# Optimization experiments

Measured on AMD Instinct MI355X. Metric: run time of the kernel, lower is better.

Reference implementation:

```python
import jax, jax.numpy as jnp
import numpy as np
import math

L = 4      # layers / experts
AD = 512   # agent dim per layer
D = 512    # wsi_size / model dim
T = 64     # num_tokens
N = 4096   # WSI patches
NC = 2
PROJ = 256 # cosine gate projection dim
HID = 4 * D
CAP = math.ceil(T / L)  # top-1, capacity_factor=1.0
EPS = 1e-5
AUX_W = 0.01


def layer_norm(x, g, b):
    x32 = x.astype(jnp.float32)
    mu = x32.mean(-1, keepdims=True)
    var = x32.var(-1, keepdims=True)
    return ((x32 - mu) * jax.lax.rsqrt(var + EPS) * g + b).astype(x.dtype)


def mha(q_in, kv_in, w_qkv, b_qkv, w_out, b_out, n_heads):
    # torch nn.MultiheadAttention, unbatched (len, embed) inputs
    E = q_in.shape[-1]
    hd = E // n_heads
    wq, wk, wv = jnp.split(w_qkv, 3, axis=0)
    bq, bk, bv = jnp.split(b_qkv, 3)
    q = (q_in @ wq.T + bq).reshape(-1, n_heads, hd)
    k = (kv_in @ wk.T + bk).reshape(-1, n_heads, hd)
    v = (kv_in @ wv.T + bv).reshape(-1, n_heads, hd)
    scale = float(1.0 / np.sqrt(hd))
    attn = jax.nn.softmax(jnp.einsum('thd,shd->hts', q, k) * scale, axis=-1)
    out = jnp.einsum('hts,shd->thd', attn, v).reshape(-1, E)
    return out @ w_out.T + b_out


def moe_top1(x, proj_w, sim_mat, temp, w1, b1, w2, b2):
    # tutel cosine top-1 gate (fp32), capacity-limited batch-prioritized dispatch
    E = w1.shape[0]
    xf = x.astype(jnp.float32)
    p = xf @ proj_w                                             # [T, PROJ]
    p = p / (jnp.linalg.norm(p, axis=-1, keepdims=True) + 1e-8)
    s = sim_mat / (jnp.linalg.norm(sim_mat, axis=0, keepdims=True) + 1e-8)
    scale = jnp.exp(jnp.minimum(temp, jnp.log(jnp.float32(100.0))))
    logits = (p @ s) * scale                                    # [T, E]
    scores = jax.nn.softmax(logits, axis=-1)
    expert = jnp.argmax(logits, axis=-1)                        # [T]
    gate = jnp.take_along_axis(scores, expert[:, None], axis=1)[:, 0]
    # batch prioritized routing: higher-gate tokens claim capacity slots first
    order = jnp.argsort(-gate)
    oh = jax.nn.one_hot(expert[order], E, dtype=jnp.int32)
    pos_s = jnp.sum(jnp.cumsum(oh, axis=0) * oh, axis=1) - 1    # slot within expert
    inv = jnp.argsort(order)
    pos = pos_s[inv]
    keep = pos < CAP
    safe_pos = jnp.where(keep, pos, 0)
    # dispatch -> grouped expert FFN -> combine
    buf = jnp.zeros((E, CAP, x.shape[-1]), x.dtype)
    buf = buf.at[expert, safe_pos].add(jnp.where(keep[:, None], x, 0.0))
    h = jax.nn.gelu(jnp.einsum('ecd,edh->ech', buf, w1) + b1[:, None, :], approximate=False)
    y = jnp.einsum('ech,ehd->ecd', h, w2) + b2[:, None, :]
    out = y[expert, safe_pos] * (gate * keep)[:, None].astype(x.dtype)
    # load-balancing aux loss (top-1)
    me = scores.mean(0)
    ce = jax.nn.one_hot(expert, E, dtype=jnp.float32).mean(0)
    l_aux = jnp.sum(me * ce) * E
    return out, l_aux


def reference(share_feature, fet_tokens, ind_ln1_g, ind_ln1_b, ind_ln2_g, ind_ln2_b,
              ind_qkv_w, ind_qkv_b, ind_out_w, ind_out_b, ind_mlp_w, ind_mlp_b,
              gate_proj_w, gate_sim, gate_temp, exp_w1, exp_b1, exp_w2, exp_b2,
              gsa_ln1_g, gsa_ln1_b, gsa_qkv_w, gsa_qkv_b, gsa_out_w, gsa_out_b,
              gsa_ln2_g, gsa_ln2_b, gsa_fc_w, gsa_fc_b, gsa_proj_w, gsa_proj_b,
              butter_w, butter_b, cls_w, cls_b):
    cur = jnp.zeros((T, D), share_feature.dtype)
    feature1 = jnp.zeros((L, T, D), share_feature.dtype)
    aux = jnp.zeros((1,), jnp.float32)
    for i in range(L):  # small fixed per-layer loop (structurally distinct params)
        seg = share_feature[:, i * AD:(i + 1) * AD]
        sf = layer_norm(seg, ind_ln1_g[i], ind_ln1_b[i])
        tok = layer_norm(fet_tokens[i], ind_ln2_g[i], ind_ln2_b[i])
        attn_out = mha(tok, sf, ind_qkv_w[i], ind_qkv_b[i], ind_out_w[i], ind_out_b[i], AD)
        qf = attn_out @ ind_mlp_w[i].T + ind_mlp_b[i]   # [T, D]
        mo, la = moe_top1(qf, gate_proj_w, gate_sim, gate_temp, exp_w1, exp_b1, exp_w2, exp_b2)
        cur = cur + mo
        aux = aux + la * AUX_W
        feature1 = feature1.at[i].set(cur)
    cur = cur / L
    # GatedSFAttentionBlock (8 heads self-attn + QuickGELU MLP, pre-LN residual)
    x1 = layer_norm(cur, gsa_ln1_g, gsa_ln1_b)
    x = cur + mha(x1, x1, gsa_qkv_w, gsa_qkv_b, gsa_out_w, gsa_out_b, D // 64)
    x2 = layer_norm(x, gsa_ln2_g, gsa_ln2_b)
    h = x2 @ gsa_fc_w.T + gsa_fc_b
    h = h * jax.nn.sigmoid(1.702 * h)  # QuickGELU
    gated = x + (h @ gsa_proj_w.T + gsa_proj_b)
    # OutputBlock
    hb = (gated @ butter_w.T + butter_b).reshape(1, -1)  # [1, T*256]
    logits = hb @ cls_w.T + cls_b                        # [1, NC]
    Y_hat = jnp.argmax(logits, axis=1, keepdims=True)
    hazards = jax.nn.sigmoid(logits)
    feature2 = jnp.zeros((L, T, D), share_feature.dtype)
    feature2_pre = jnp.zeros((L, 1, NC), share_feature.dtype)
    return (logits, hazards, Y_hat, aux, feature1, feature2, feature2_pre)


def setup_inputs() -> dict:
    key = jax.random.key(0)
    ks = iter(jax.random.split(key, 40))
    def rn(shape, scale=0.02):
        return scale * jax.random.normal(next(ks), shape, dtype=jnp.float32)
    return dict(
        share_feature=jax.random.normal(next(ks), (N, L * AD), dtype=jnp.float32),
        fet_tokens=rn((L, T, AD), AD ** -0.5),
        ind_ln1_g=jnp.ones((L, AD)), ind_ln1_b=jnp.zeros((L, AD)),
        ind_ln2_g=jnp.ones((L, AD)), ind_ln2_b=jnp.zeros((L, AD)),
        ind_qkv_w=rn((L, 3 * AD, AD)), ind_qkv_b=jnp.zeros((L, 3 * AD)),
        ind_out_w=rn((L, AD, AD)), ind_out_b=jnp.zeros((L, AD)),
        ind_mlp_w=rn((L, D, AD)), ind_mlp_b=jnp.zeros((L, D)),
        gate_proj_w=rn((D, PROJ)), gate_sim=rn((PROJ, L)),
        gate_temp=jnp.asarray(np.log(10.0), jnp.float32),
        exp_w1=rn((L, D, HID)), exp_b1=jnp.zeros((L, HID)),
        exp_w2=rn((L, HID, D)), exp_b2=jnp.zeros((L, D)),
        gsa_ln1_g=jnp.ones((D,)), gsa_ln1_b=jnp.zeros((D,)),
        gsa_qkv_w=rn((3 * D, D)), gsa_qkv_b=jnp.zeros((3 * D,)),
        gsa_out_w=rn((D, D)), gsa_out_b=jnp.zeros((D,)),
        gsa_ln2_g=jnp.ones((D,)), gsa_ln2_b=jnp.zeros((D,)),
        gsa_fc_w=rn((4 * D, D)), gsa_fc_b=jnp.zeros((4 * D,)),
        gsa_proj_w=rn((D, 4 * D)), gsa_proj_b=jnp.zeros((D,)),
        butter_w=rn((256, D)), butter_b=jnp.zeros((256,)),
        cls_w=rn((NC, T * 256)), cls_b=jnp.zeros((NC,)),
    )
```

## Files before the change

### kernel.cpp

```cpp
#include <hip/hip_runtime.h>
#include <math.h>

#define LNUM 4
#define ADIM 512
#define TTOK 64
#define NSEQ 4096
#define HIDE 2048
#define CAPE 16
#define EPSV 1e-5f

typedef __bf16 bf16;
typedef bf16 bf16x8 __attribute__((ext_vector_type(8)));
typedef float f32x4 __attribute__((ext_vector_type(4)));

#define OFF_BUF   0
#define OFF_SSUM  (OFF_BUF  + 131072)
#define OFF_CNT   (OFF_SSUM + 16)
#define OFF_Q     (OFF_CNT  + 16)
#define OFF_AP    (OFF_Q    + 131072)
#define OFF_QF    (OFF_AP   + 131072)
#define OFF_P     (OFF_QF   + 131072)
#define OFF_QKV3  (OFF_P    + 65536)
#define OFF_XB    (OFF_QKV3 + 98304)
#define OFF_HROW  (OFF_XB   + 32768)
#define OFF_GTD   (OFF_HROW + 131072)
#define OFF_HB    (OFF_GTD  + 32768)
#define ZERO_N    (OFF_HB   + 16384)
#define OFF_KT    ZERO_N
#define OFF_VT    (OFF_KT   + LNUM*512*NSEQ)
#define OFF_KMAX  (OFF_VT   + LNUM*512*NSEQ)
#define OFF_KMIN  (OFF_KMAX + LNUM*512)
#define OFF_AO    (OFF_KMIN + LNUM*512)
#define OFF_GATE  (OFF_AO   + 131072)
#define OFF_EXP   (OFF_GATE + 256)
#define OFF_POS   (OFF_EXP  + 256)
#define OFF_KEEP  (OFF_POS  + 256)
#define OFF_HEXP  (OFF_KEEP + 256)
#define OFF_CUR   (OFF_HEXP + LNUM*4*CAPE*HIDE)
#define OFF_AO2   (OFF_CUR  + TTOK*512)
#define OFF_AH    (OFF_AO2  + TTOK*512)
#define OFF_AL    (OFF_AH + LNUM*NSEQ*256)
#define OFF_WH    (OFF_AL + LNUM*NSEQ*256)
#define OFF_WL    (OFF_WH + LNUM*1024*256)
#define OFF_YEXP  OFF_AH

#define O_F1   6
#define O_F2   (6 + LNUM*TTOK*512)
#define O_F2P  (O_F2 + LNUM*TTOK*512)

__device__ __forceinline__ float wave_sum(float v) {
#pragma unroll
  for (int o = 32; o > 0; o >>= 1) v += __shfl_down(v, o, 64);
  return v;
}
__device__ __forceinline__ float wave_sum_all(float v) {
#pragma unroll
  for (int o = 32; o > 0; o >>= 1) v += __shfl_xor(v, o, 64);
  return v;
}
__device__ __forceinline__ float block_sum256(float v) {
  __shared__ float r[4];
  v = wave_sum(v);
  int wid = threadIdx.x >> 6, lane = threadIdx.x & 63;
  if (lane == 0) r[wid] = v;
  __syncthreads();
  float s = r[0] + r[1] + r[2] + r[3];
  __syncthreads();
  return s;
}

__global__ void k_zero(float* __restrict__ p, int n) {
  int i = blockIdx.x * 256 + threadIdx.x;
  if (i < n) p[i] = 0.f;
}

__global__ __launch_bounds__(64) void k_cvt_a(const float* __restrict__ SF,
      const float* __restrict__ G, const float* __restrict__ Bta,
      bf16* __restrict__ AH, bf16* __restrict__ AL) {
  int row = blockIdx.x;
  int l = row >> 12, m = row & 4095;
  int lane = threadIdx.x;
  const float* src = SF + (size_t)m * (LNUM * ADIM) + l * ADIM;
  float4 a = *(const float4*)(src + lane * 8);
  float4 b = *(const float4*)(src + lane * 8 + 4);
  float sum = (a.x + a.y) + (a.z + a.w) + (b.x + b.y) + (b.z + b.w);
  float sq = a.x*a.x + a.y*a.y + a.z*a.z + a.w*a.w + b.x*b.x + b.y*b.y + b.z*b.z + b.w*b.w;
  sum = wave_sum_all(sum); sq = wave_sum_all(sq);
  float mu = sum * (1.f / 512.f);
  float rs = rsqrtf(sq * (1.f / 512.f) - mu * mu + EPSV);
  float4 g0 = *(const float4*)(G + l * 512 + lane * 8);
  float4 g1 = *(const float4*)(G + l * 512 + lane * 8 + 4);
  float4 c0 = *(const float4*)(Bta + l * 512 + lane * 8);
  float4 c1 = *(const float4*)(Bta + l * 512 + lane * 8 + 4);
  float x[8];
  x[0] = (a.x - mu) * rs * g0.x + c0.x;  x[1] = (a.y - mu) * rs * g0.y + c0.y;
  x[2] = (a.z - mu) * rs * g0.z + c0.z;  x[3] = (a.w - mu) * rs * g0.w + c0.w;
  x[4] = (b.x - mu) * rs * g1.x + c1.x;  x[5] = (b.y - mu) * rs * g1.y + c1.y;
  x[6] = (b.z - mu) * rs * g1.z + c1.z;  x[7] = (b.w - mu) * rs * g1.w + c1.w;
  bf16x8 vh, vl;
#pragma unroll
  for (int j = 0; j < 8; j++) {
    bf16 h = (bf16)x[j];
    vh[j] = h;
    vl[j] = (bf16)(x[j] - (float)h);
  }
  *(bf16x8*)(AH + (size_t)row * 512 + lane * 8) = vh;
  *(bf16x8*)(AL + (size_t)row * 512 + lane * 8) = vl;
}

__global__ __launch_bounds__(64) void k_cvt_w(const float* __restrict__ Wqkv,
      bf16* __restrict__ WH, bf16* __restrict__ WL) {
  int row = blockIdx.x;
  int l = row >> 10, r = row & 1023;
  int lane = threadIdx.x;
  const float* src = Wqkv + (size_t)l * 1536 * 512 + (size_t)(512 + r) * 512 + lane * 8;
  float4 a = *(const float4*)(src);
  float4 b = *(const float4*)(src + 4);
  float x[8] = {a.x, a.y, a.z, a.w, b.x, b.y, b.z, b.w};
  bf16x8 vh, vl;
#pragma unroll
  for (int j = 0; j < 8; j++) {
    bf16 h = (bf16)x[j];
    vh[j] = h;
    vl[j] = (bf16)(x[j] - (float)h);
  }
  *(bf16x8*)(WH + (size_t)row * 512 + lane * 8) = vh;
  *(bf16x8*)(WL + (size_t)row * 512 + lane * 8) = vl;
}

__global__ __launch_bounds__(256) void k_mfma_kv(
      const bf16* __restrict__ AH, const bf16* __restrict__ AL,
      const bf16* __restrict__ WH, const bf16* __restrict__ WL,
      const float* __restrict__ Bqkv,
      float* __restrict__ KT, float* __restrict__ VT) {
  __shared__ bf16 sAh[128*32], sAl[128*32], sWh[128*32], sWl[128*32];
  int l = blockIdx.z;
  int n0 = blockIdx.x * 128, m0 = blockIdx.y * 128;
  int tid = threadIdx.x;
  int lane = tid & 63;
  int w = tid >> 6;
  int wm = w >> 1, wn = w & 1;
  const bf16* gAh = AH + ((size_t)l * 4096 + m0) * 512;
  const bf16* gAl = AL + ((size_t)l * 4096 + m0) * 512;
  const bf16* gWh = WH + ((size_t)l * 1024 + n0) * 512;
  const bf16* gWl = WL + ((size_t)l * 1024 + n0) * 512;
  int ch0 = tid * 2, ch1 = tid * 2 + 1;
  int r0 = ch0 >> 2, q0 = (ch0 & 3) * 8;
  int r1 = ch1 >> 2, q1 = (ch1 & 3) * 8;
  int fr = lane & 15, fq = (lane >> 4) * 8;
  f32x4 acc[4][4] = {};
  for (int k0 = 0; k0 < 512; k0 += 32) {
    *(bf16x8*)&sAh[r0*32 + q0] = *(const bf16x8*)&gAh[(size_t)r0*512 + k0 + q0];
    *(bf16x8*)&sAh[r1*32 + q1] = *(const bf16x8*)&gAh[(size_t)r1*512 + k0 + q1];
    *(bf16x8*)&sAl[r0*32 + q0] = *(const bf16x8*)&gAl[(size_t)r0*512 + k0 + q0];
    *(bf16x8*)&sAl[r1*32 + q1] = *(const bf16x8*)&gAl[(size_t)r1*512 + k0 + q1];
    *(bf16x8*)&sWh[r0*32 + q0] = *(const bf16x8*)&gWh[(size_t)r0*512 + k0 + q0];
    *(bf16x8*)&sWh[r1*32 + q1] = *(const bf16x8*)&gWh[(size_t)r1*512 + k0 + q1];
    *(bf16x8*)&sWl[r0*32 + q0] = *(const bf16x8*)&gWl[(size_t)r0*512 + k0 + q0];
    *(bf16x8*)&sWl[r1*32 + q1] = *(const bf16x8*)&gWl[(size_t)r1*512 + k0 + q1];
    __syncthreads();
    bf16x8 ah[4], al[4], bh[4], bl[4];
#pragma unroll
    for (int i = 0; i < 4; i++) {
      ah[i] = *(const bf16x8*)&sAh[(wm*64 + i*16 + fr)*32 + fq];
      al[i] = *(const bf16x8*)&sAl[(wm*64 + i*16 + fr)*32 + fq];
      bh[i] = *(const bf16x8*)&sWh[(wn*64 + i*16 + fr)*32 + fq];
      bl[i] = *(const bf16x8*)&sWl[(wn*64 + i*16 + fr)*32 + fq];
    }
#pragma unroll
    for (int i = 0; i < 4; i++)
#pragma unroll
      for (int j = 0; j < 4; j++) {
        acc[i][j] = __builtin_amdgcn_mfma_f32_16x16x32_bf16(ah[i], bh[j], acc[i][j], 0, 0, 0);
        acc[i][j] = __builtin_amdgcn_mfma_f32_16x16x32_bf16(ah[i], bl[j], acc[i][j], 0, 0, 0);
        acc[i][j] = __builtin_amdgcn_mfma_f32_16x16x32_bf16(al[i], bh[j], acc[i][j], 0, 0, 0);
      }
    __syncthreads();
  }
#pragma unroll
  for (int j = 0; j < 4; j++) {
    int n = n0 + wn*64 + j*16 + fr;
    float bias = Bqkv[l * 1536 + 512 + n];
    float* base = (n < 512) ? (KT + ((size_t)(l*512 + n)) * 4096)
                            : (VT + ((size_t)(l*512 + n - 512)) * 4096);
#pragma unroll
    for (int i = 0; i < 4; i++) {
      int mb = m0 + wm*64 + i*16 + (lane >> 4) * 4;
      float4 o = make_float4(acc[i][j][0] + bias, acc[i][j][1] + bias,
                             acc[i][j][2] + bias, acc[i][j][3] + bias);
      *(float4*)(base + mb) = o;
    }
  }
}

__global__ __launch_bounds__(256) void k_minmax(const float* __restrict__ KT,
                                                float* __restrict__ kmax, float* __restrict__ kmin) {
  int row = blockIdx.x;
  const float4* k = (const float4*)(KT + (size_t)row * 4096);
  float mx = -3.4e38f, mn = 3.4e38f;
  for (int i = threadIdx.x; i < 1024; i += 256) {
    float4 v = k[i];
    mx = fmaxf(mx, fmaxf(fmaxf(v.x, v.y), fmaxf(v.z, v.w)));
    mn = fminf(mn, fminf(fminf(v.x, v.y), fminf(v.z, v.w)));
  }
#pragma unroll
  for (int o = 32; o > 0; o >>= 1) {
    mx = fmaxf(mx, __shfl_down(mx, o, 64));
    mn = fminf(mn, __shfl_down(mn, o, 64));
  }
  __shared__ float rmx[4], rmn[4];
  int wid = threadIdx.x >> 6, lane = threadIdx.x & 63;
  if (lane == 0) { rmx[wid] = mx; rmn[wid] = mn; }
  __syncthreads();
  if (threadIdx.x == 0) {
    kmax[row] = fmaxf(fmaxf(rmx[0], rmx[1]), fmaxf(rmx[2], rmx[3]));
    kmin[row] = fminf(fminf(rmn[0], rmn[1]), fminf(rmn[2], rmn[3]));
  }
}

__global__ __launch_bounds__(64) void k_ln(const float* __restrict__ IN,
      const float* __restrict__ G, const float* __restrict__ B,
      float* __restrict__ OUT, int gstride) {
  int t = blockIdx.x, l = blockIdx.y;
  int row = l * 64 + t;
  int lane = threadIdx.x;
  const float* x = IN + (size_t)row * 512 + lane * 8;
  float4 a = ((const float4*)x)[0], b = ((const float4*)x)[1];
  float sum = (a.x + a.y) + (a.z + a.w) + (b.x + b.y) + (b.z + b.w);
  float sq = a.x*a.x + a.y*a.y + a.z*a.z + a.w*a.w + b.x*b.x + b.y*b.y + b.z*b.z + b.w*b.w;
  sum = wave_sum_all(sum); sq = wave_sum_all(sq);
  float mu = sum * (1.f / 512.f);
  float rs = rsqrtf(sq * (1.f / 512.f) - mu * mu + EPSV);
  const float* gp = G + l * gstride + lane * 8;
  const float* bp = B + l * gstride + lane * 8;
  float4 g0 = ((const float4*)gp)[0], g1 = ((const float4*)gp)[1];
  float4 c0 = ((const float4*)bp)[0], c1 = ((const float4*)bp)[1];
  float4 o0, o1;
  o0.x = (a.x - mu) * rs * g0.x + c0.x;  o0.y = (a.y - mu) * rs * g0.y + c0.y;
  o0.z = (a.z - mu) * rs * g0.z + c0.z;  o0.w = (a.w - mu) * rs * g0.w + c0.w;
  o1.x = (b.x - mu) * rs * g1.x + c1.x;  o1.y = (b.y - mu) * rs * g1.y + c1.y;
  o1.z = (b.z - mu) * rs * g1.z + c1.z;  o1.w = (b.w - mu) * rs * g1.w + c1.w;
  float* op = OUT + (size_t)row * 512 + lane * 8;
  ((float4*)op)[0] = o0; ((float4*)op)[1] = o1;
}

__global__ __launch_bounds__(256) void k_gemm64(
      const float* __restrict__ IN, const float* __restrict__ W,
      const float* __restrict__ BIAS, const float* __restrict__ RES,
      float* __restrict__ OUT, int K, int N, long wl, int bl) {
  int l = blockIdx.z;
  int n0 = blockIdx.x * 64;
  int kc0 = blockIdx.y * 128;
  const float* INl = IN + (size_t)l * 64 * K;
  const float* Wl  = W + (size_t)l * wl;
  float* OUTl = OUT + (size_t)l * 64 * N;
  __shared__ float sA[64][68], sB[64][68];
  int tid = threadIdx.x;
  int tx = tid & 15, ty = tid >> 4;
  float acc[4][4];
  if (blockIdx.y == 0) {
#pragma unroll
    for (int j = 0; j < 4; j++) {
      float bv = BIAS ? BIAS[bl * l + n0 + tx*4 + j] : 0.f;
#pragma unroll
      for (int i = 0; i < 4; i++)
        acc[i][j] = bv + (RES ? RES[((size_t)l*64 + ty*4 + i) * N + n0 + tx*4 + j] : 0.f);
    }
  } else {
#pragma unroll
    for (int i = 0; i < 4; i++)
#pragma unroll
      for (int j = 0; j < 4; j++) acc[i][j] = 0.f;
  }
  for (int kc = kc0; kc < kc0 + 128; kc += 64) {
    for (int i = tid; i < 1024; i += 256) {
      int r = i >> 4;
      int kq = i & 15;
      float4 av = *(const float4*)(INl + (size_t)r * K + kc + kq*4);
      sA[kq*4+0][r] = av.x; sA[kq*4+1][r] = av.y; sA[kq*4+2][r] = av.z; sA[kq*4+3][r] = av.w;
      float4 bv = *(const float4*)(Wl + (size_t)(n0 + r) * K + kc + kq*4);
      sB[kq*4+0][r] = bv.x; sB[kq*4+1][r] = bv.y; sB[kq*4+2][r] = bv.z; sB[kq*4+3][r] = bv.w;
    }
    __syncthreads();
#pragma unroll 8
    for (int kk = 0; kk < 64; kk++) {
      float4 a4 = *(const float4*)&sA[kk][ty*4];
      float4 b4 = *(const float4*)&sB[kk][tx*4];
      float a[4] = {a4.x,a4.y,a4.z,a4.w}, b[4] = {b4.x,b4.y,b4.z,b4.w};
#pragma unroll
      for (int i = 0; i < 4; i++)
#pragma unroll
        for (int j = 0; j < 4; j++) acc[i][j] = fmaf(a[i], b[j], acc[i][j]);
    }
    __syncthreads();
  }
#pragma unroll
  for (int i = 0; i < 4; i++)
#pragma unroll
    for (int j = 0; j < 4; j++)
      atomicAdd(&OUTl[(size_t)(ty*4+i) * N + n0 + tx*4 + j], acc[i][j]);
}

__global__ __launch_bounds__(256) void k_gemm64t(
      const float* __restrict__ IN, const float* __restrict__ W,
      float* __restrict__ OUT, int K, int N) {
  int l = blockIdx.z;
  int n0 = blockIdx.x * 64;
  int kc0 = blockIdx.y * 128;
  const float* INl = IN + (size_t)l * 64 * K;
  float* OUTl = OUT + (size_t)l * 64 * N;
  __shared__ float sA[64][68], sB[64][68];
  int tid = threadIdx.x;
  int tx = tid & 15, ty = tid >> 4;
  float acc[4][4] = {};
  for (int kc = kc0; kc < kc0 + 128; kc += 64) {
    for (int i = tid; i < 1024; i += 256) {
      int r = i >> 4;
      int kq = i & 15;
      float4 av = *(const float4*)(INl + (size_t)r * K + kc + kq*4);
      sA[kq*4+0][r] = av.x; sA[kq*4+1][r] = av.y; sA[kq*4+2][r] = av.z; sA[kq*4+3][r] = av.w;
      float4 bv = *(const float4*)(W + (size_t)(kc + r) * N + n0 + kq*4);
      *(float4*)&sB[r][kq*4] = bv;
    }
    __syncthreads();
#pragma unroll 8
    for (int kk = 0; kk < 64; kk++) {
      float4 a4 = *(const float4*)&sA[kk][ty*4];
      float4 b4 = *(const float4*)&sB[kk][tx*4];
      float a[4] = {a4.x,a4.y,a4.z,a4.w}, b[4] = {b4.x,b4.y,b4.z,b4.w};
#pragma unroll
      for (int i = 0; i < 4; i++)
#pragma unroll
        for (int j = 0; j < 4; j++) acc[i][j] = fmaf(a[i], b[j], acc[i][j]);
    }
    __syncthreads();
  }
#pragma unroll
  for (int i = 0; i < 4; i++)
#pragma unroll
    for (int j = 0; j < 4; j++)
      atomicAdd(&OUTl[(size_t)(ty*4+i) * N + n0 + tx*4 + j], acc[i][j]);
}

__global__ __launch_bounds__(256) void k_attn(const float* __restrict__ KT, const float* __restrict__ VT,
      const float* __restrict__ Q, const float* __restrict__ kmax, const float* __restrict__ kmin,
      float* __restrict__ AO) {
  int h = blockIdx.x, l = blockIdx.y;
  int tid = threadIdx.x;
  int w = tid >> 6, t = tid & 63;
  __shared__ float pden[4][64], pnum[4][64];
  const float* kp = KT + ((size_t)(l * 512 + h)) * 4096 + w * 1024;
  const float* vp = VT + ((size_t)(l * 512 + h)) * 4096 + w * 1024;
  float q = Q[((size_t)l * TTOK + t) * 512 + h];
  float km = kmax[l * 512 + h], kn = kmin[l * 512 + h];
  float m = (q >= 0.f) ? q * km : q * kn;
  float d0 = 0.f, d1 = 0.f, n0 = 0.f, n1 = 0.f;
  for (int s = 0; s < 1024; s += 8) {
    float4 ka = *(const float4*)(kp + s), kb = *(const float4*)(kp + s + 4);
    float4 va = *(const float4*)(vp + s), vb = *(const float4*)(vp + s + 4);
    float e;
    e = __expf(fmaf(q, ka.x, -m)); d0 += e; n0 = fmaf(e, va.x, n0);
    e = __expf(fmaf(q, ka.y, -m)); d1 += e; n1 = fmaf(e, va.y, n1);
    e = __expf(fmaf(q, ka.z, -m)); d0 += e; n0 = fmaf(e, va.z, n0);
    e = __expf(fmaf(q, ka.w, -m)); d1 += e; n1 = fmaf(e, va.w, n1);
    e = __expf(fmaf(q, kb.x, -m)); d0 += e; n0 = fmaf(e, vb.x, n0);
    e = __expf(fmaf(q, kb.y, -m)); d1 += e; n1 = fmaf(e, vb.y, n1);
    e = __expf(fmaf(q, kb.z, -m)); d0 += e; n0 = fmaf(e, vb.z, n0);
    e = __expf(fmaf(q, kb.w, -m)); d1 += e; n1 = fmaf(e, vb.w, n1);
  }
  pden[w][t] = d0 + d1; pnum[w][t] = n0 + n1;
  __syncthreads();
  if (w == 0) {
    float d = pden[0][t] + pden[1][t] + pden[2][t] + pden[3][t];
    float n = pnum[0][t] + pnum[1][t] + pnum[2][t] + pnum[3][t];
    AO[((size_t)l * TTOK + t) * 512 + h] = n / d;
  }
}

__global__ __launch_bounds__(64) void k_gate2(const float* __restrict__ P,
      const float* __restrict__ SIM, const float* __restrict__ TEMP,
      float* __restrict__ gate, int* __restrict__ expert,
      float* __restrict__ ssum, int* __restrict__ cnt) {
  int t = blockIdx.x, l = blockIdx.y;
  int lane = threadIdx.x;
  float4 p4 = *(const float4*)(P + ((size_t)(l * 64 + t)) * 256 + lane * 4);
  float ss = p4.x*p4.x + p4.y*p4.y + p4.z*p4.z + p4.w*p4.w;
  ss = wave_sum_all(ss);
  float invp = 1.f / (sqrtf(ss) + 1e-8f);
  float le[4] = {}, ne[4] = {};
#pragma unroll
  for (int j = 0; j < 4; j++) {
    float pv = (j == 0) ? p4.x : (j == 1) ? p4.y : (j == 2) ? p4.z : p4.w;
    float4 s4 = *(const float4*)(SIM + (size_t)(lane * 4 + j) * 4);
    le[0] = fmaf(pv, s4.x, le[0]); le[1] = fmaf(pv, s4.y, le[1]);
    le[2] = fmaf(pv, s4.z, le[2]); le[3] = fmaf(pv, s4.w, le[3]);
    ne[0] = fmaf(s4.x, s4.x, ne[0]); ne[1] = fmaf(s4.y, s4.y, ne[1]);
    ne[2] = fmaf(s4.z, s4.z, ne[2]); ne[3] = fmaf(s4.w, s4.w, ne[3]);
  }
#pragma unroll
  for (int e = 0; e < 4; e++) { le[e] = wave_sum_all(le[e]); ne[e] = wave_sum_all(ne[e]); }
  if (lane == 0) {
    float scale = __expf(fminf(TEMP[0], 4.6051701859880914f));
    float lg[4];
#pragma unroll
    for (int e = 0; e < 4; e++) lg[e] = le[e] * invp / (sqrtf(ne[e]) + 1e-8f) * scale;
    int best = 0; float bv = lg[0];
    if (lg[1] > bv) { best = 1; bv = lg[1]; }
    if (lg[2] > bv) { best = 2; bv = lg[2]; }
    if (lg[3] > bv) { best = 3; bv = lg[3]; }
    float mx = fmaxf(fmaxf(lg[0], lg[1]), fmaxf(lg[2], lg[3]));
    float e0 = __expf(lg[0]-mx), e1 = __expf(lg[1]-mx), e2 = __expf(lg[2]-mx), e3 = __expf(lg[3]-mx);
    float inv = 1.f / (e0 + e1 + e2 + e3);
    float s0 = e0*inv, s1 = e1*inv, s2 = e2*inv, s3 = e3*inv;
    float sb = (best == 0) ? s0 : (best == 1) ? s1 : (best == 2) ? s2 : s3;
    gate[l * TTOK + t] = sb;
    expert[l * TTOK + t] = best;
    atomicAdd(&ssum[l*4+0], s0); atomicAdd(&ssum[l*4+1], s1);
    atomicAdd(&ssum[l*4+2], s2); atomicAdd(&ssum[l*4+3], s3);
    atomicAdd(&cnt[l*4+best], 1);
  }
}

__global__ __launch_bounds__(64) void k_route(const float* __restrict__ gate, const int* __restrict__ expert,
                                              int* __restrict__ pos, int* __restrict__ keep) {
  int l = blockIdx.x;
  int t = threadIdx.x;
  __shared__ float g[64];
  __shared__ int e[64];
  g[t] = gate[l * TTOK + t]; e[t] = expert[l * TTOK + t];
  __syncthreads();
  float gt = g[t]; int et = e[t];
  int p = 0;
  for (int u = 0; u < 64; u++)
    if (e[u] == et && (g[u] > gt || (g[u] == gt && u < t))) p++;
  pos[l * TTOK + t] = p;
  keep[l * TTOK + t] = (p < CAPE) ? 1 : 0;
}

__global__ __launch_bounds__(128) void k_scatter(const float* __restrict__ QF, const int* __restrict__ expert,
      const int* __restrict__ pos, const int* __restrict__ keep, float* __restrict__ buf) {
  int t = blockIdx.x, l = blockIdx.y;
  int idx = l * TTOK + t;
  if (!keep[idx]) return;
  int e = expert[idx], p = pos[idx];
  const float4* src = (const float4*)(QF + ((size_t)l * TTOK + t) * 512);
  float4* dst = (float4*)(buf + (((size_t)(l * 4 + e)) * CAPE + p) * 512);
  dst[threadIdx.x] = src[threadIdx.x];
}

__global__ __launch_bounds__(256) void k_moe_h(const float* __restrict__ buf, const float* __restrict__ W1,
      const float* __restrict__ B1, float* __restrict__ H) {
  int le = blockIdx.y;
  int e = le & 3;
  int col = blockIdx.x * 256 + threadIdx.x;
  const float* act = buf + (size_t)le * 16 * 512;
  const float* wp = W1 + (size_t)e * 512 * HIDE + col;
  float acc[16];
#pragma unroll
  for (int c = 0; c < 16; c++) acc[c] = 0.f;
  for (int k0 = 0; k0 < 512; k0 += 4) {
    float4 a[16];
#pragma unroll
    for (int c = 0; c < 16; c++) a[c] = *(const float4*)(act + c * 512 + k0);
#pragma unroll
    for (int j = 0; j < 4; j++) {
      float wv = wp[(size_t)(k0 + j) * HIDE];
#pragma unroll
      for (int c = 0; c < 16; c++) acc[c] = fmaf(((const float*)&a[c])[j], wv, acc[c]);
    }
  }
  float bias = B1[e * HIDE + col];
  float* outp = H + (size_t)le * 16 * HIDE + col;
#pragma unroll
  for (int c = 0; c < 16; c++) {
    float v = acc[c] + bias;
    outp[(size_t)c * HIDE] = 0.5f * v * (1.f + erff(v * 0.70710678118654752f));
  }
}

__global__ __launch_bounds__(256) void k_moe_y(const float* __restrict__ H, const float* __restrict__ W2,
      const float* __restrict__ B2, float* __restrict__ Y) {
  int le = blockIdx.y;
  int e = le & 3;
  int cl = threadIdx.x & 63, kq = threadIdx.x >> 6;
  int col = blockIdx.x * 64 + cl;
  const float* act = H + (size_t)le * 16 * HIDE + kq * 512;
  const float* wp = W2 + (size_t)e * HIDE * 512 + (size_t)(kq * 512) * 512 + col;
  float acc[16];
#pragma unroll
  for (int c = 0; c < 16; c++) acc[c] = 0.f;
  for (int k0 = 0; k0 < 512; k0 += 4) {
    float4 a[16];
#pragma unroll
    for (int c = 0; c < 16; c++) a[c] = *(const float4*)(act + c * HIDE + k0);
#pragma unroll
    for (int j = 0; j < 4; j++) {
      float wv = wp[(size_t)(k0 + j) * 512];
#pragma unroll
      for (int c = 0; c < 16; c++) acc[c] = fmaf(((const float*)&a[c])[j], wv, acc[c]);
    }
  }
  __shared__ float sacc[4][16][64];
#pragma unroll
  for (int c = 0; c < 16; c++) sacc[kq][c][cl] = acc[c];
  __syncthreads();
  if (kq == 0) {
    float bias = B2[e * 512 + col];
#pragma unroll
    for (int c = 0; c < 16; c++) {
      float tot = sacc[0][c][cl] + sacc[1][c][cl] + sacc[2][c][cl] + sacc[3][c][cl] + bias;
      Y[(size_t)le * 16 * 512 + (size_t)c * 512 + col] = tot;
    }
  }
}

__global__ __launch_bounds__(512) void k_combine(const float* __restrict__ Y, const int* __restrict__ expert,
      const int* __restrict__ pos, const int* __restrict__ keep, const float* __restrict__ gate,
      float* __restrict__ f1, float* __restrict__ f2, float* __restrict__ cur) {
  int t = blockIdx.x;
  int d = threadIdx.x;
  float acc = 0.f;
#pragma unroll
  for (int l = 0; l < LNUM; l++) {
    int idx = l * TTOK + t;
    float v = 0.f;
    if (keep[idx]) {
      int e = expert[idx], p = pos[idx];
      v = Y[(((size_t)(l * 4 + e)) * CAPE + p) * 512 + d] * gate[idx];
    }
    acc += v;
    f1[((size_t)l * TTOK + t) * 512 + d] = acc;
    f2[((size_t)l * TTOK + t) * 512 + d] = 0.f;
  }
  cur[(size_t)t * 512 + d] = acc * 0.25f;
}

__global__ __launch_bounds__(256) void k_gsa_attn(const float* __restrict__ QKV3, float* __restrict__ AO2) {
  int h = blockIdx.x;
  __shared__ float qh[64][65], kh[64][65], vh[64][65];
  __shared__ float ps[4][64];
  for (int i = threadIdx.x; i < 4096; i += 256) {
    int t = i >> 6, d = i & 63;
    qh[t][d] = QKV3[(size_t)t * 1536 + h * 64 + d];
    kh[t][d] = QKV3[(size_t)t * 1536 + 512 + h * 64 + d];
    vh[t][d] = QKV3[(size_t)t * 1536 + 1024 + h * 64 + d];
  }
  __syncthreads();
  int w = threadIdx.x >> 6, lane = threadIdx.x & 63;
  for (int tt = 0; tt < 16; tt++) {
    int t = w * 16 + tt;
    float acc = 0.f;
#pragma unroll 8
    for (int d = 0; d < 64; d++) acc = fmaf(qh[t][d], kh[lane][d], acc);
    acc *= 0.125f;
    float m = acc;
#pragma unroll
    for (int o = 32; o > 0; o >>= 1) m = fmaxf(m, __shfl_xor(m, o, 64));
    float e = __expf(acc - m);
    float den = e;
#pragma unroll
    for (int o = 32; o > 0; o >>= 1) den += __shfl_xor(den, o, 64);
    ps[w][lane] = e / den;
    __syncthreads();
    float o2 = 0.f;
#pragma unroll 8
    for (int s = 0; s < 64; s++) o2 = fmaf(ps[w][s], vh[s][lane], o2);
    AO2[(size_t)t * 512 + h * 64 + lane] = o2;
    __syncthreads();
  }
}

__global__ __launch_bounds__(256) void k_swish(float* __restrict__ H) {
  int i = blockIdx.x * 256 + threadIdx.x;
  float x = H[i];
  H[i] = x / (1.f + __expf(-1.702f * x));
}

__global__ __launch_bounds__(256) void k_final(const float* __restrict__ HB,
      const float* __restrict__ CW, const float* __restrict__ CB,
      const float* __restrict__ ssum, const int* __restrict__ cnt,
      float* __restrict__ out) {
  int tid = threadIdx.x;
  float p0 = 0.f, p1 = 0.f;
  for (int i = tid; i < 16384; i += 256) {
    float h = HB[i];
    p0 = fmaf(h, CW[i], p0);
    p1 = fmaf(h, CW[16384 + i], p1);
  }
  p0 = block_sum256(p0);
  p1 = block_sum256(p1);
  if (tid == 0) {
    float l0 = p0 + CB[0], l1 = p1 + CB[1];
    out[0] = l0; out[1] = l1;
    out[2] = 1.f / (1.f + __expf(-l0));
    out[3] = 1.f / (1.f + __expf(-l1));
    out[4] = (l1 > l0) ? 1.f : 0.f;
    float aux = 0.f;
    for (int i = 0; i < 16; i++) aux += (ssum[i] * (1.f / 64.f)) * ((float)cnt[i] * (1.f / 64.f));
    out[5] = aux * 4.f * 0.01f;
  }
  if (tid < 8) out[O_F2P + tid] = 0.f;
}

extern "C" void kernel_launch(void* const* d_in, const int* in_sizes, int n_in,
                              void* d_out, int out_size, void* d_ws, size_t ws_size,
                              hipStream_t stream) {
  const float* SF    = (const float*)d_in[0];
  const float* TOK   = (const float*)d_in[1];
  const float* LN1G  = (const float*)d_in[2];
  const float* LN1B  = (const float*)d_in[3];
  const float* LN2G  = (const float*)d_in[4];
  const float* LN2B  = (const float*)d_in[5];
  const float* QKVW  = (const float*)d_in[6];
  const float* QKVB  = (const float*)d_in[7];
  const float* OUTW  = (const float*)d_in[8];
  const float* OUTB  = (const float*)d_in[9];
  const float* MLPW  = (const float*)d_in[10];
  const float* MLPB  = (const float*)d_in[11];
  const float* GPW   = (const float*)d_in[12];
  const float* GSIM  = (const float*)d_in[13];
  const float* GTMP  = (const float*)d_in[14];
  const float* EW1   = (const float*)d_in[15];
  const float* EB1   = (const float*)d_in[16];
  const float* EW2   = (const float*)d_in[17];
  const float* EB2   = (const float*)d_in[18];
  const float* GL1G  = (const float*)d_in[19];
  const float* GL1B  = (const float*)d_in[20];
  const float* GQKVW = (const float*)d_in[21];
  const float* GQKVB = (const float*)d_in[22];
  const float* GOUTW = (const float*)d_in[23];
  const float* GOUTB = (const float*)d_in[24];
  const float* GL2G  = (const float*)d_in[25];
  const float* GL2B  = (const float*)d_in[26];
  const float* GFCW  = (const float*)d_in[27];
  const float* GFCB  = (const float*)d_in[28];
  const float* GPJW  = (const float*)d_in[29];
  const float* GPJB  = (const float*)d_in[30];
  const float* BTW   = (const float*)d_in[31];
  const float* BTB   = (const float*)d_in[32];
  const float* CLW   = (const float*)d_in[33];
  const float* CLB   = (const float*)d_in[34];

  float* ws  = (float*)d_ws;
  float* out = (float*)d_out;

  float* BUF  = ws + OFF_BUF;
  float* SSUM = ws + OFF_SSUM;
  int*   CNT  = (int*)(ws + OFF_CNT);
  float* Q    = ws + OFF_Q;
  float* AP   = ws + OFF_AP;
  float* QF   = ws + OFF_QF;
  float* P    = ws + OFF_P;
  float* QKV3 = ws + OFF_QKV3;
  float* XB   = ws + OFF_XB;
  float* HROW = ws + OFF_HROW;
  float* GTD  = ws + OFF_GTD;
  float* HBB  = ws + OFF_HB;
  float* KT   = ws + OFF_KT;
  float* VT   = ws + OFF_VT;
  float* KMAX = ws + OFF_KMAX;
  float* KMIN = ws + OFF_KMIN;
  float* AOSH = ws + OFF_AO;
  float* GATE = ws + OFF_GATE;
  int*   EXPI = (int*)(ws + OFF_EXP);
  int*   POSI = (int*)(ws + OFF_POS);
  int*   KEEPI= (int*)(ws + OFF_KEEP);
  float* HEXP = ws + OFF_HEXP;
  float* CUR  = ws + OFF_CUR;
  float* AO2  = ws + OFF_AO2;
  bf16*  AH   = (bf16*)(ws + OFF_AH);
  bf16*  AL   = (bf16*)(ws + OFF_AL);
  bf16*  WH   = (bf16*)(ws + OFF_WH);
  bf16*  WL   = (bf16*)(ws + OFF_WL);
  float* YEXP = ws + OFF_YEXP;

  k_zero<<<(ZERO_N + 255) / 256, 256, 0, stream>>>(ws, ZERO_N);
  k_cvt_a<<<LNUM * NSEQ, 64, 0, stream>>>(SF, LN1G, LN1B, AH, AL);
  k_cvt_w<<<LNUM * 1024, 64, 0, stream>>>(QKVW, WH, WL);
  k_mfma_kv<<<dim3(8, 32, LNUM), 256, 0, stream>>>(AH, AL, WH, WL, QKVB, KT, VT);
  k_minmax<<<LNUM * 512, 256, 0, stream>>>(KT, KMAX, KMIN);
  k_ln<<<dim3(TTOK, LNUM), 64, 0, stream>>>(TOK, LN2G, LN2B, AOSH, 512);
  k_gemm64<<<dim3(8, 4, LNUM), 256, 0, stream>>>(AOSH, QKVW, QKVB, nullptr, Q, 512, 512, 1536L*512, 1536);
  k_attn<<<dim3(512, LNUM), 256, 0, stream>>>(KT, VT, Q, KMAX, KMIN, AOSH);
  k_gemm64<<<dim3(8, 4, LNUM), 256, 0, stream>>>(AOSH, OUTW, OUTB, nullptr, AP, 512, 512, 512L*512, 512);
  k_gemm64<<<dim3(8, 4, LNUM), 256, 0, stream>>>(AP, MLPW, MLPB, nullptr, QF, 512, 512, 512L*512, 512);
  k_gemm64t<<<dim3(4, 4, LNUM), 256, 0, stream>>>(QF, GPW, P, 512, 256);
  k_gate2<<<dim3(TTOK, LNUM), 64, 0, stream>>>(P, GSIM, GTMP, GATE, EXPI, SSUM, CNT);
  k_route<<<LNUM, 64, 0, stream>>>(GATE, EXPI, POSI, KEEPI);
  k_scatter<<<dim3(TTOK, LNUM), 128, 0, stream>>>(QF, EXPI, POSI, KEEPI, BUF);
  k_moe_h<<<dim3(8, 16), 256, 0, stream>>>(BUF, EW1, EB1, HEXP);
  k_moe_y<<<dim3(8, 16), 256, 0, stream>>>(HEXP, EW2, EB2, YEXP);
  k_combine<<<TTOK, 512, 0, stream>>>(YEXP, EXPI, POSI, KEEPI, GATE, out + O_F1, out + O_F2, CUR);
  k_ln<<<dim3(TTOK, 1), 64, 0, stream>>>(CUR, GL1G, GL1B, AOSH, 0);
  k_gemm64<<<dim3(24, 4, 1), 256, 0, stream>>>(AOSH, GQKVW, GQKVB, nullptr, QKV3, 512, 1536, 0, 0);
  k_gsa_attn<<<8, 256, 0, stream>>>(QKV3, AO2);
  k_gemm64<<<dim3(8, 4, 1), 256, 0, stream>>>(AO2, GOUTW, GOUTB, CUR, XB, 512, 512, 0, 0);
  k_ln<<<dim3(TTOK, 1), 64, 0, stream>>>(XB, GL2G, GL2B, AOSH, 0);
  k_gemm64<<<dim3(32, 4, 1), 256, 0, stream>>>(AOSH, GFCW, GFCB, nullptr, HROW, 512, 2048, 0, 0);
  k_swish<<<(TTOK * HIDE) / 256, 256, 0, stream>>>(HROW);
  k_gemm64<<<dim3(8, 16, 1), 256, 0, stream>>>(HROW, GPJW, GPJB, XB, GTD, 2048, 512, 0, 0);
  k_gemm64<<<dim3(4, 4, 1), 256, 0, stream>>>(GTD, BTW, BTB, nullptr, HBB, 512, 256, 0, 0);
  k_final<<<1, 256, 0, stream>>>(HBB, CLW, CLB, SSUM, CNT, out);
}
```

Baseline: 818.3 us.

## Fuse min/max into attention, merge MoE gating kernels, fuse swish into GEMM

Computes K min/max inside the attention kernel, which now keeps K/V in registers and loops over tokens with exp2, so the separate min/max pass and its extra read of K are gone. Merges the gate, route and scatter kernels into one per-layer block. Fuses swish into a non-split GEMM epilogue, removing the separate swish kernel. Also swaps the MFMA grid axes to change block scheduling order. Fewer launches and less memory traffic, at the cost of less parallelism in the fused gate kernel and the unsplit FC GEMM.

```diff
diff --git a/kernel.cpp b/kernel.cpp
--- a/kernel.cpp
+++ b/kernel.cpp
@@ -8,6 +8,7 @@
 #define HIDE 2048
 #define CAPE 16
 #define EPSV 1e-5f
+#define LOG2E 1.44269504088896340736f
 
 typedef __bf16 bf16;
 typedef bf16 bf16x8 __attribute__((ext_vector_type(8)));
@@ -28,9 +29,7 @@
 #define ZERO_N    (OFF_HB   + 16384)
 #define OFF_KT    ZERO_N
 #define OFF_VT    (OFF_KT   + LNUM*512*NSEQ)
-#define OFF_KMAX  (OFF_VT   + LNUM*512*NSEQ)
-#define OFF_KMIN  (OFF_KMAX + LNUM*512)
-#define OFF_AO    (OFF_KMIN + LNUM*512)
+#define OFF_AO    (OFF_VT   + LNUM*512*NSEQ)
 #define OFF_GATE  (OFF_AO   + 131072)
 #define OFF_EXP   (OFF_GATE + 256)
 #define OFF_POS   (OFF_EXP  + 256)
@@ -135,7 +134,7 @@
       float* __restrict__ KT, float* __restrict__ VT) {
   __shared__ bf16 sAh[128*32], sAl[128*32], sWh[128*32], sWl[128*32];
   int l = blockIdx.z;
-  int n0 = blockIdx.x * 128, m0 = blockIdx.y * 128;
+  int m0 = blockIdx.x * 128, n0 = blockIdx.y * 128;
   int tid = threadIdx.x;
   int lane = tid & 63;
   int w = tid >> 6;
@@ -190,31 +189,6 @@
                              acc[i][j][2] + bias, acc[i][j][3] + bias);
       *(float4*)(base + mb) = o;
     }
-  }
-}
-
-__global__ __launch_bounds__(256) void k_minmax(const float* __restrict__ KT,
-                                                float* __restrict__ kmax, float* __restrict__ kmin) {
-  int row = blockIdx.x;
-  const float4* k = (const float4*)(KT + (size_t)row * 4096);
-  float mx = -3.4e38f, mn = 3.4e38f;
-  for (int i = threadIdx.x; i < 1024; i += 256) {
-    float4 v = k[i];
-    mx = fmaxf(mx, fmaxf(fmaxf(v.x, v.y), fmaxf(v.z, v.w)));
-    mn = fminf(mn, fminf(fminf(v.x, v.y), fminf(v.z, v.w)));
-  }
-#pragma unroll
-  for (int o = 32; o > 0; o >>= 1) {
-    mx = fmaxf(mx, __shfl_down(mx, o, 64));
-    mn = fminf(mn, __shfl_down(mn, o, 64));
-  }
-  __shared__ float rmx[4], rmn[4];
-  int wid = threadIdx.x >> 6, lane = threadIdx.x & 63;
-  if (lane == 0) { rmx[wid] = mx; rmn[wid] = mn; }
-  __syncthreads();
-  if (threadIdx.x == 0) {
-    kmax[row] = fmaxf(fmaxf(rmx[0], rmx[1]), fmaxf(rmx[2], rmx[3]));
-    kmin[row] = fminf(fminf(rmn[0], rmn[1]), fminf(rmn[2], rmn[3]));
   }
 }
 
@@ -247,10 +221,12 @@
 __global__ __launch_bounds__(256) void k_gemm64(
       const float* __restrict__ IN, const float* __restrict__ W,
       const float* __restrict__ BIAS, const float* __restrict__ RES,
-      float* __restrict__ OUT, int K, int N, long wl, int bl) {
+      float* __restrict__ OUT, int K, int N, long wl, int bl, int act) {
   int l = blockIdx.z;
   int n0 = blockIdx.x * 64;
-  int kc0 = blockIdx.y * 128;
+  bool split = (gridDim.y > 1);
+  int kcBeg = blockIdx.y * 128;
+  int kcEnd = split ? kcBeg + 128 : K;
   const float* INl = IN + (size_t)l * 64 * K;
   const float* Wl  = W + (size_t)l * wl;
   float* OUTl = OUT + (size_t)l * 64 * N;
@@ -272,7 +248,7 @@
 #pragma unroll
       for (int j = 0; j < 4; j++) acc[i][j] = 0.f;
   }
-  for (int kc = kc0; kc < kc0 + 128; kc += 64) {
+  for (int kc = kcBeg; kc < kcEnd; kc += 64) {
     for (int i = tid; i < 1024; i += 256) {
       int r = i >> 4;
       int kq = i & 15;
@@ -294,11 +270,22 @@
     }
     __syncthreads();
   }
-#pragma unroll
-  for (int i = 0; i < 4; i++)
-#pragma unroll
-    for (int j = 0; j < 4; j++)
-      atomicAdd(&OUTl[(size_t)(ty*4+i) * N + n0 + tx*4 + j], acc[i][j]);
+  if (split) {
+#pragma unroll
+    for (int i = 0; i < 4; i++)
+#pragma unroll
+      for (int j = 0; j < 4; j++)
+        atomicAdd(&OUTl[(size_t)(ty*4+i) * N + n0 + tx*4 + j], acc[i][j]);
+  } else {
+#pragma unroll
+    for (int i = 0; i < 4; i++)
+#pragma unroll
+      for (int j = 0; j < 4; j++) {
+        float o = acc[i][j];
+        if (act == 1) o = o / (1.f + __expf(-1.702f * o));
+        OUTl[(size_t)(ty*4+i) * N + n0 + tx*4 + j] = o;
+      }
+  }
 }
 
 __global__ __launch_bounds__(256) void k_gemm64t(
@@ -343,63 +330,102 @@
 }
 
 __global__ __launch_bounds__(256) void k_attn(const float* __restrict__ KT, const float* __restrict__ VT,
-      const float* __restrict__ Q, const float* __restrict__ kmax, const float* __restrict__ kmin,
-      float* __restrict__ AO) {
+      const float* __restrict__ Q, float* __restrict__ AO) {
   int h = blockIdx.x, l = blockIdx.y;
   int tid = threadIdx.x;
-  int w = tid >> 6, t = tid & 63;
-  __shared__ float pden[4][64], pnum[4][64];
-  const float* kp = KT + ((size_t)(l * 512 + h)) * 4096 + w * 1024;
-  const float* vp = VT + ((size_t)(l * 512 + h)) * 4096 + w * 1024;
-  float q = Q[((size_t)l * TTOK + t) * 512 + h];
-  float km = kmax[l * 512 + h], kn = kmin[l * 512 + h];
-  float m = (q >= 0.f) ? q * km : q * kn;
-  float d0 = 0.f, d1 = 0.f, n0 = 0.f, n1 = 0.f;
-  for (int s = 0; s < 1024; s += 8) {
-    float4 ka = *(const float4*)(kp + s), kb = *(const float4*)(kp + s + 4);
-    float4 va = *(const float4*)(vp + s), vb = *(const float4*)(vp + s + 4);
-    float e;
-    e = __expf(fmaf(q, ka.x, -m)); d0 += e; n0 = fmaf(e, va.x, n0);
-    e = __expf(fmaf(q, ka.y, -m)); d1 += e; n1 = fmaf(e, va.y, n1);
-    e = __expf(fmaf(q, ka.z, -m)); d0 += e; n0 = fmaf(e, va.z, n0);
-    e = __expf(fmaf(q, ka.w, -m)); d1 += e; n1 = fmaf(e, va.w, n1);
-    e = __expf(fmaf(q, kb.x, -m)); d0 += e; n0 = fmaf(e, vb.x, n0);
-    e = __expf(fmaf(q, kb.y, -m)); d1 += e; n1 = fmaf(e, vb.y, n1);
-    e = __expf(fmaf(q, kb.z, -m)); d0 += e; n0 = fmaf(e, vb.z, n0);
-    e = __expf(fmaf(q, kb.w, -m)); d1 += e; n1 = fmaf(e, vb.w, n1);
-  }
-  pden[w][t] = d0 + d1; pnum[w][t] = n0 + n1;
+  int w = tid >> 6, lane = tid & 63;
+  __shared__ float2 sacc[4][16][65];
+  __shared__ float wmx[4], wmn[4];
+  size_t base = ((size_t)(l * 512 + h)) * 4096 + w * 1024;
+  float kv[16], vv[16];
+#pragma unroll
+  for (int c = 0; c < 4; c++) {
+    *(float4*)&kv[c*4] = *(const float4*)(KT + base + c * 256 + lane * 4);
+    *(float4*)&vv[c*4] = *(const float4*)(VT + base + c * 256 + lane * 4);
+  }
+  float mx = kv[0], mn = kv[0];
+#pragma unroll
+  for (int i = 1; i < 16; i++) { mx = fmaxf(mx, kv[i]); mn = fminf(mn, kv[i]); }
+#pragma unroll
+  for (int o = 32; o > 0; o >>= 1) {
+    mx = fmaxf(mx, __shfl_xor(mx, o, 64));
+    mn = fminf(mn, __shfl_xor(mn, o, 64));
+  }
+  if (lane == 0) { wmx[w] = mx; wmn[w] = mn; }
   __syncthreads();
-  if (w == 0) {
-    float d = pden[0][t] + pden[1][t] + pden[2][t] + pden[3][t];
-    float n = pnum[0][t] + pnum[1][t] + pnum[2][t] + pnum[3][t];
-    AO[((size_t)l * TTOK + t) * 512 + h] = n / d;
-  }
-}
-
-__global__ __launch_bounds__(64) void k_gate2(const float* __restrict__ P,
+  float km = fmaxf(fmaxf(wmx[0], wmx[1]), fmaxf(wmx[2], wmx[3]));
+  float kn = fminf(fminf(wmn[0], wmn[1]), fminf(wmn[2], wmn[3]));
+  float q_own = Q[((size_t)l * TTOK + lane) * 512 + h];
+  float q2_own = q_own * LOG2E;
+  float m2_own = ((q_own >= 0.f) ? q_own * km : q_own * kn) * LOG2E;
+  int rt = tid >> 4, rj = tid & 15;
+  for (int cc = 0; cc < 4; cc++) {
+    for (int tt = 0; tt < 16; tt++) {
+      int t = cc * 16 + tt;
+      float q2t = __shfl(q2_own, t, 64);
+      float m2t = __shfl(m2_own, t, 64);
+      float den = 0.f, num = 0.f;
+#pragma unroll
+      for (int i = 0; i < 16; i++) {
+        float e = exp2f(fmaf(q2t, kv[i], -m2t));
+        den += e;
+        num = fmaf(e, vv[i], num);
+      }
+      sacc[w][tt][lane] = make_float2(den, num);
+    }
+    __syncthreads();
+    float2 a = make_float2(0.f, 0.f);
+#pragma unroll
+    for (int g = 0; g < 4; g++)
+#pragma unroll
+      for (int s4 = 0; s4 < 4; s4++) {
+        float2 v = sacc[g][rt][rj + 16 * s4];
+        a.x += v.x; a.y += v.y;
+      }
+#pragma unroll
+    for (int o = 8; o > 0; o >>= 1) {
+      a.x += __shfl_down(a.x, o, 16);
+      a.y += __shfl_down(a.y, o, 16);
+    }
+    if (rj == 0) {
+      int t = cc * 16 + rt;
+      AO[((size_t)l * TTOK + t) * 512 + h] = a.y / a.x;
+    }
+    __syncthreads();
+  }
+}
+
+__global__ __launch_bounds__(256) void k_moe_gate(const float* __restrict__ P,
       const float* __restrict__ SIM, const float* __restrict__ TEMP,
+      const float* __restrict__ QF,
       float* __restrict__ gate, int* __restrict__ expert,
-      float* __restrict__ ssum, int* __restrict__ cnt) {
-  int t = blockIdx.x, l = blockIdx.y;
-  int lane = threadIdx.x;
-  float4 p4 = *(const float4*)(P + ((size_t)(l * 64 + t)) * 256 + lane * 4);
-  float ss = p4.x*p4.x + p4.y*p4.y + p4.z*p4.z + p4.w*p4.w;
-  ss = wave_sum_all(ss);
-  float invp = 1.f / (sqrtf(ss) + 1e-8f);
-  float le[4] = {}, ne[4] = {};
-#pragma unroll
-  for (int j = 0; j < 4; j++) {
-    float pv = (j == 0) ? p4.x : (j == 1) ? p4.y : (j == 2) ? p4.z : p4.w;
-    float4 s4 = *(const float4*)(SIM + (size_t)(lane * 4 + j) * 4);
+      int* __restrict__ pos, int* __restrict__ keep,
+      float* __restrict__ ssum, int* __restrict__ cnt, float* __restrict__ buf) {
+  int l = blockIdx.x;
+  int tid = threadIdx.x;
+  int t = tid >> 2, q = tid & 3;
+  __shared__ float score_s[4][64];
+  __shared__ float g_s[64];
+  __shared__ int e_s[64], keep_s[64], pos_s[64];
+  const float* prow = P + ((size_t)(l * 64 + t)) * 256 + q * 64;
+  float ss = 0.f, le[4] = {}, ne[4] = {};
+  for (int j = 0; j < 64; j++) {
+    float pv = prow[j];
+    ss = fmaf(pv, pv, ss);
+    float4 s4 = *(const float4*)(SIM + (size_t)(q * 64 + j) * 4);
     le[0] = fmaf(pv, s4.x, le[0]); le[1] = fmaf(pv, s4.y, le[1]);
     le[2] = fmaf(pv, s4.z, le[2]); le[3] = fmaf(pv, s4.w, le[3]);
     ne[0] = fmaf(s4.x, s4.x, ne[0]); ne[1] = fmaf(s4.y, s4.y, ne[1]);
     ne[2] = fmaf(s4.z, s4.z, ne[2]); ne[3] = fmaf(s4.w, s4.w, ne[3]);
   }
 #pragma unroll
-  for (int e = 0; e < 4; e++) { le[e] = wave_sum_all(le[e]); ne[e] = wave_sum_all(ne[e]); }
-  if (lane == 0) {
+  for (int o = 2; o > 0; o >>= 1) {
+    ss += __shfl_xor(ss, o, 4);
+#pragma unroll
+    for (int e = 0; e < 4; e++) { le[e] += __shfl_xor(le[e], o, 4); ne[e] += __shfl_xor(ne[e], o, 4); }
+  }
+  if (q == 0) {
+    float invp = 1.f / (sqrtf(ss) + 1e-8f);
     float scale = __expf(fminf(TEMP[0], 4.6051701859880914f));
     float lg[4];
 #pragma unroll
@@ -411,41 +437,37 @@
     float mx = fmaxf(fmaxf(lg[0], lg[1]), fmaxf(lg[2], lg[3]));
     float e0 = __expf(lg[0]-mx), e1 = __expf(lg[1]-mx), e2 = __expf(lg[2]-mx), e3 = __expf(lg[3]-mx);
     float inv = 1.f / (e0 + e1 + e2 + e3);
-    float s0 = e0*inv, s1 = e1*inv, s2 = e2*inv, s3 = e3*inv;
-    float sb = (best == 0) ? s0 : (best == 1) ? s1 : (best == 2) ? s2 : s3;
+    score_s[0][t] = e0*inv; score_s[1][t] = e1*inv; score_s[2][t] = e2*inv; score_s[3][t] = e3*inv;
+    float sb = score_s[best][t];
+    g_s[t] = sb; e_s[t] = best;
     gate[l * TTOK + t] = sb;
     expert[l * TTOK + t] = best;
-    atomicAdd(&ssum[l*4+0], s0); atomicAdd(&ssum[l*4+1], s1);
-    atomicAdd(&ssum[l*4+2], s2); atomicAdd(&ssum[l*4+3], s3);
-    atomicAdd(&cnt[l*4+best], 1);
-  }
-}
-
-__global__ __launch_bounds__(64) void k_route(const float* __restrict__ gate, const int* __restrict__ expert,
-                                              int* __restrict__ pos, int* __restrict__ keep) {
-  int l = blockIdx.x;
-  int t = threadIdx.x;
-  __shared__ float g[64];
-  __shared__ int e[64];
-  g[t] = gate[l * TTOK + t]; e[t] = expert[l * TTOK + t];
+  }
   __syncthreads();
-  float gt = g[t]; int et = e[t];
-  int p = 0;
-  for (int u = 0; u < 64; u++)
-    if (e[u] == et && (g[u] > gt || (g[u] == gt && u < t))) p++;
-  pos[l * TTOK + t] = p;
-  keep[l * TTOK + t] = (p < CAPE) ? 1 : 0;
-}
-
-__global__ __launch_bounds__(128) void k_scatter(const float* __restrict__ QF, const int* __restrict__ expert,
-      const int* __restrict__ pos, const int* __restrict__ keep, float* __restrict__ buf) {
-  int t = blockIdx.x, l = blockIdx.y;
-  int idx = l * TTOK + t;
-  if (!keep[idx]) return;
-  int e = expert[idx], p = pos[idx];
-  const float4* src = (const float4*)(QF + ((size_t)l * TTOK + t) * 512);
-  float4* dst = (float4*)(buf + (((size_t)(l * 4 + e)) * CAPE + p) * 512);
-  dst[threadIdx.x] = src[threadIdx.x];
+  if (tid < 64) {
+    float gt = g_s[tid]; int et = e_s[tid];
+    int p = 0;
+    for (int u = 0; u < 64; u++)
+      if (e_s[u] == et && (g_s[u] > gt || (g_s[u] == gt && u < tid))) p++;
+    pos_s[tid] = p; keep_s[tid] = (p < CAPE) ? 1 : 0;
+    pos[l * TTOK + tid] = p;
+    keep[l * TTOK + tid] = (p < CAPE) ? 1 : 0;
+  } else if (tid < 68) {
+    int e = tid - 64;
+    float s = 0.f; int c = 0;
+    for (int u = 0; u < 64; u++) { s += score_s[e][u]; c += (e_s[u] == e); }
+    ssum[l * 4 + e] = s;
+    cnt[l * 4 + e] = c;
+  }
+  __syncthreads();
+  int which = tid >> 7, idx = tid & 127;
+  for (int tb = 0; tb < 64; tb += 2) {
+    int tt = tb + which;
+    if (keep_s[tt]) {
+      float4* dst = (float4*)(buf + (((size_t)(l * 4 + e_s[tt])) * CAPE + pos_s[tt]) * 512);
+      dst[idx] = ((const float4*)(QF + ((size_t)l * TTOK + tt) * 512))[idx];
+    }
+  }
 }
 
 __global__ __launch_bounds__(256) void k_moe_h(const float* __restrict__ buf, const float* __restrict__ W1,
@@ -568,12 +590,6 @@
     AO2[(size_t)t * 512 + h * 64 + lane] = o2;
     __syncthreads();
   }
-}
-
-__global__ __launch_bounds__(256) void k_swish(float* __restrict__ H) {
-  int i = blockIdx.x * 256 + threadIdx.x;
-  float x = H[i];
-  H[i] = x / (1.f + __expf(-1.702f * x));
 }
 
 __global__ __launch_bounds__(256) void k_final(const float* __restrict__ HB,
@@ -658,8 +674,6 @@
   float* HBB  = ws + OFF_HB;
   float* KT   = ws + OFF_KT;
   float* VT   = ws + OFF_VT;
-  float* KMAX = ws + OFF_KMAX;
-  float* KMIN = ws + OFF_KMIN;
   float* AOSH = ws + OFF_AO;
   float* GATE = ws + OFF_GATE;
   int*   EXPI = (int*)(ws + OFF_EXP);
@@ -677,28 +691,24 @@
   k_zero<<<(ZERO_N + 255) / 256, 256, 0, stream>>>(ws, ZERO_N);
   k_cvt_a<<<LNUM * NSEQ, 64, 0, stream>>>(SF, LN1G, LN1B, AH, AL);
   k_cvt_w<<<LNUM * 1024, 64, 0, stream>>>(QKVW, WH, WL);
-  k_mfma_kv<<<dim3(8, 32, LNUM), 256, 0, stream>>>(AH, AL, WH, WL, QKVB, KT, VT);
-  k_minmax<<<LNUM * 512, 256, 0, stream>>>(KT, KMAX, KMIN);
+  k_mfma_kv<<<dim3(32, 8, LNUM), 256, 0, stream>>>(AH, AL, WH, WL, QKVB, KT, VT);
   k_ln<<<dim3(TTOK, LNUM), 64, 0, stream>>>(TOK, LN2G, LN2B, AOSH, 512);
-  k_gemm64<<<dim3(8, 4, LNUM), 256, 0, stream>>>(AOSH, QKVW, QKVB, nullptr, Q, 512, 512, 1536L*512, 1536);
-  k_attn<<<dim3(512, LNUM), 256, 0, stream>>>(KT, VT, Q, KMAX, KMIN, AOSH);
-  k_gemm64<<<dim3(8, 4, LNUM), 256, 0, stream>>>(AOSH, OUTW, OUTB, nullptr, AP, 512, 512, 512L*512, 512);
-  k_gemm64<<<dim3(8, 4, LNUM), 256, 0, stream>>>(AP, MLPW, MLPB, nullptr, QF, 512, 512, 512L*512, 512);
+  k_gemm64<<<dim3(8, 4, LNUM), 256, 0, stream>>>(AOSH, QKVW, QKVB, nullptr, Q, 512, 512, 1536L*512, 1536, 0);
+  k_attn<<<dim3(512, LNUM), 256, 0, stream>>>(KT, VT, Q, AOSH);
+  k_gemm64<<<dim3(8, 4, LNUM), 256, 0, stream>>>(AOSH, OUTW, OUTB, nullptr, AP, 512, 512, 512L*512, 512, 0);
+  k_gemm64<<<dim3(8, 4, LNUM), 256, 0, stream>>>(AP, MLPW, MLPB, nullptr, QF, 512, 512, 512L*512, 512, 0);
   k_gemm64t<<<dim3(4, 4, LNUM), 256, 0, stream>>>(QF, GPW, P, 512, 256);
-  k_gate2<<<dim3(TTOK, LNUM), 64, 0, stream>>>(P, GSIM, GTMP, GATE, EXPI, SSUM, CNT);
-  k_route<<<LNUM, 64, 0, stream>>>(GATE, EXPI, POSI, KEEPI);
-  k_scatter<<<dim3(TTOK, LNUM), 128, 0, stream>>>(QF, EXPI, POSI, KEEPI, BUF);
+  k_moe_gate<<<LNUM, 256, 0, stream>>>(P, GSIM, GTMP, QF, GATE, EXPI, POSI, KEEPI, SSUM, CNT, BUF);
   k_moe_h<<<dim3(8, 16), 256, 0, stream>>>(BUF, EW1, EB1, HEXP);
   k_moe_y<<<dim3(8, 16), 256, 0, stream>>>(HEXP, EW2, EB2, YEXP);
   k_combine<<<TTOK, 512, 0, stream>>>(YEXP, EXPI, POSI, KEEPI, GATE, out + O_F1, out + O_F2, CUR);
   k_ln<<<dim3(TTOK, 1), 64, 0, stream>>>(CUR, GL1G, GL1B, AOSH, 0);
-  k_gemm64<<<dim3(24, 4, 1), 256, 0, stream>>>(AOSH, GQKVW, GQKVB, nullptr, QKV3, 512, 1536, 0, 0);
+  k_gemm64<<<dim3(24, 4, 1), 256, 0, stream>>>(AOSH, GQKVW, GQKVB, nullptr, QKV3, 512, 1536, 0, 0, 0);
   k_gsa_attn<<<8, 256, 0, stream>>>(QKV3, AO2);
-  k_gemm64<<<dim3(8, 4, 1), 256, 0, stream>>>(AO2, GOUTW, GOUTB, CUR, XB, 512, 512, 0, 0);
+  k_gemm64<<<dim3(8, 4, 1), 256, 0, stream>>>(AO2, GOUTW, GOUTB, CUR, XB, 512, 512, 0, 0, 0);
   k_ln<<<dim3(TTOK, 1), 64, 0, stream>>>(XB, GL2G, GL2B, AOSH, 0);
-  k_gemm64<<<dim3(32, 4, 1), 256, 0, stream>>>(AOSH, GFCW, GFCB, nullptr, HROW, 512, 2048, 0, 0);
-  k_swish<<<(TTOK * HIDE) / 256, 256, 0, stream>>>(HROW);
-  k_gemm64<<<dim3(8, 16, 1), 256, 0, stream>>>(HROW, GPJW, GPJB, XB, GTD, 2048, 512, 0, 0);
-  k_gemm64<<<dim3(4, 4, 1), 256, 0, stream>>>(GTD, BTW, BTB, nullptr, HBB, 512, 256, 0, 0);
+  k_gemm64<<<dim3(32, 1, 1), 256, 0, stream>>>(AOSH, GFCW, GFCB, nullptr, HROW, 512, 2048, 0, 0, 1);
+  k_gemm64<<<dim3(8, 16, 1), 256, 0, stream>>>(HROW, GPJW, GPJB, XB, GTD, 2048, 512, 0, 0, 0);
+  k_gemm64<<<dim3(4, 4, 1), 256, 0, stream>>>(GTD, BTW, BTB, nullptr, HBB, 512, 256, 0, 0, 0);
   k_final<<<1, 256, 0, stream>>>(HBB, CLW, CLB, SSUM, CNT, out);
 }
```

Result: slower. 838.0 us (+2.4%).
